# Kernel tuning notes

Measured on AMD Instinct MI355X. Metric: run time of the kernel, lower is better.

Reference implementation:

```python
import jax, jax.numpy as jnp
import numpy as np

B, S, D, H, HD = 2, 4096, 1024, 16, 64   # batch, seq, hidden, heads, head_dim
BLOCK, W = 64, 8                          # block size, local window in blocks (512 tokens)
ROPE_BASE = 10000.0


def _rope_tables(seq_len, dim, dtype):
    inv_freq = 1.0 / (ROPE_BASE ** (jnp.arange(0, dim, 2, dtype=jnp.float32) / dim))
    t = jnp.arange(seq_len, dtype=jnp.float32)
    freqs = jnp.einsum('i,j->ij', t, inv_freq)          # [S, dim/2]
    emb = jnp.concatenate([freqs, freqs], axis=-1)       # [S, dim]
    return jnp.cos(emb).astype(dtype), jnp.sin(emb).astype(dtype)


def _rotate_half(x):
    x1, x2 = x[..., : x.shape[-1] // 2], x[..., x.shape[-1] // 2:]
    return jnp.concatenate([-x2, x1], axis=-1)


def _apply_rope(q, k, position_ids):
    # q, k: [B, H, S, HD]; position_ids: [B, S]
    cos_t, sin_t = _rope_tables(S, HD, q.dtype)
    cos = cos_t[position_ids][:, None, :, :]             # [B, 1, S, HD]
    sin = sin_t[position_ids][:, None, :, :]
    q_emb = q * cos + _rotate_half(q) * sin
    k_emb = k * cos + _rotate_half(k) * sin
    return q_emb, k_emb


def _block_sparse_attention(q, k, v):
    # Causal block-sparse (sliding window of W blocks), DeepSpeed-style layout.
    # q, k, v: [B, H, S, HD]
    nb = S // BLOCK
    scale = 1.0 / jnp.sqrt(jnp.asarray(HD, q.dtype))
    qb = q.reshape(B, H, nb, BLOCK, HD)
    kb = k.reshape(B, H, nb, BLOCK, HD)
    vb = v.reshape(B, H, nb, BLOCK, HD)
    # block-column indices attended by each block-row: i-W+1 .. i
    idx = jnp.arange(nb)[:, None] - jnp.arange(W - 1, -1, -1)[None, :]   # [nb, W]
    valid = idx >= 0
    idxc = jnp.clip(idx, 0, nb - 1)
    kg = kb[:, :, idxc]                                   # [B, H, nb, W, BLOCK, HD]
    vg = vb[:, :, idxc]
    scores = jnp.einsum('bhnqd,bhnwkd->bhnqwk', qb, kg) * scale  # [B,H,nb,BLOCK,W,BLOCK]
    # absolute positions for causal mask within the window
    qpos = (jnp.arange(nb) * BLOCK)[:, None, None, None] + jnp.arange(BLOCK)[None, :, None, None]  # [nb,BLOCK,1,1]
    kpos = (idxc * BLOCK)[:, None, :, None] + jnp.arange(BLOCK)[None, None, None, :]               # [nb,1,W,BLOCK]
    mask = (kpos <= qpos) & valid[:, None, :, None]       # [nb, BLOCK, W, BLOCK]
    neg = jnp.asarray(-1e9, scores.dtype)
    scores = jnp.where(mask[None, None], scores, neg)
    scores = scores.reshape(B, H, nb, BLOCK, W * BLOCK)
    probs = jax.nn.softmax(scores, axis=-1)
    out = jnp.einsum('bhnqk,bhnkd->bhnqd', probs, vg.reshape(B, H, nb, W * BLOCK, HD))
    return out.reshape(B, H, S, HD)


def setup_inputs() -> dict:
    key = jax.random.key(0)
    ks = jax.random.split(key, 5)
    hidden_states = jax.random.normal(ks[0], (B, S, D), dtype=jnp.float32)
    position_ids = jnp.tile(jnp.arange(S, dtype=jnp.int32)[None, :], (B, 1))
    w_init = lambda k: (jax.random.normal(k, (D, D), dtype=jnp.float32) * 0.02)
    return {
        'hidden_states': hidden_states,
        'position_ids': position_ids,
        'wq': w_init(ks[1]),  # stored [in, out]
        'wk': w_init(ks[2]),
        'wv': w_init(ks[3]),
        'wo': w_init(ks[4]),
    }


def reference(hidden_states, position_ids, wq, wk, wv, wo):
    q = jnp.einsum('bsd,de->bse', hidden_states, wq).reshape(B, S, H, HD).transpose(0, 2, 1, 3)
    k = jnp.einsum('bsd,de->bse', hidden_states, wk).reshape(B, S, H, HD).transpose(0, 2, 1, 3)
    v = jnp.einsum('bsd,de->bse', hidden_states, wv).reshape(B, S, H, HD).transpose(0, 2, 1, 3)
    q, k = _apply_rope(q, k, position_ids)
    attn = _block_sparse_attention(q, k, v)               # [B, H, S, HD]
    attn = attn.transpose(0, 2, 1, 3).reshape(B, S, D)
    return jnp.einsum('bsd,de->bse', attn, wo)
```

## Files before the change

kernel.cpp:

```cpp
#include <hip/hip_runtime.h>
#include <cstdint>
#include <cstddef>

#define B_ 2
#define S_ 4096
#define D_ 1024
#define H_ 16
#define HD_ 64
#define NB_ 64
#define W_ 8
#define M_ (B_*S_)

#define QSCALE 0.18033688011112042f
#define LOG2_10000_OVER_32 0.41524101186092034f

typedef __bf16 bf16_t;
typedef __bf16 bf16x8 __attribute__((ext_vector_type(8)));
typedef float f32x4 __attribute__((ext_vector_type(4)));

#define GLOAD_LDS16(gp, lp) \
  __builtin_amdgcn_global_load_lds((__attribute__((address_space(1))) void*)(gp), \
                                   (__attribute__((address_space(3))) void*)(lp), 16, 0, 0)

__global__ void cast_bf16_kernel(const float* __restrict__ x, bf16_t* __restrict__ y, int n4) {
  int i = blockIdx.x * 256 + threadIdx.x;
  if (i >= n4) return;
  float4 v = ((const float4*)x)[i];
  union { bf16_t b[4]; uint2 u; } cv;
  cv.b[0] = (bf16_t)v.x; cv.b[1] = (bf16_t)v.y; cv.b[2] = (bf16_t)v.z; cv.b[3] = (bf16_t)v.w;
  ((uint2*)y)[i] = cv.u;
}

__global__ void transpose_cast_kernel(const float* __restrict__ w0, const float* __restrict__ w1,
                                      const float* __restrict__ w2, const float* __restrict__ w3,
                                      bf16_t* __restrict__ out) {
  const float* w = (blockIdx.z == 0) ? w0 : (blockIdx.z == 1) ? w1 : (blockIdx.z == 2) ? w2 : w3;
  bf16_t* wt = out + (size_t)blockIdx.z * D_ * D_;
  __shared__ float tile[32][33];
  int x = blockIdx.x * 32 + threadIdx.x;
  int y0 = blockIdx.y * 32;
  for (int i = threadIdx.y; i < 32; i += 8)
    tile[i][threadIdx.x] = w[(size_t)(y0 + i) * D_ + x];
  __syncthreads();
  int x2 = blockIdx.y * 32 + threadIdx.x;
  int y2 = blockIdx.x * 32;
  for (int i = threadIdx.y; i < 32; i += 8)
    wt[(size_t)(y2 + i) * D_ + x2] = (bf16_t)tile[threadIdx.x][i];
}

__global__ __launch_bounds__(512, 2) void gemm_qkv256(const bf16_t* __restrict__ A,
                                                      const bf16_t* __restrict__ Bt,
                                                      bf16_t* __restrict__ qkv,
                                                      bf16_t* __restrict__ vt_out,
                                                      const int* __restrict__ pos_ids) {
  const int bid = blockIdx.x;
  const int sid = (bid & 7) * 48 + (bid >> 3);
  const int mb = sid / 12, nb = sid % 12;
  const int mbase = mb * 256, nbase = nb * 256;
  const int tid = threadIdx.x;
  const int wid = tid >> 6, lane = tid & 63;
  const int quad = lane >> 4, l16 = lane & 15;
  const int wr = wid >> 2, wc = wid & 3;

  __shared__ bf16_t lds[4 * 16384];

  const int srow = wid * 16 + (lane >> 2);
  const int scol = (lane & 3) * 8;
  const bf16_t* gAb = A  + (size_t)(mbase + srow) * D_ + scol;
  const bf16_t* gBb = Bt + (size_t)(nbase + srow) * D_ + scol;

#define LDSA(b) (lds + (b) * 16384)
#define LDSB(b) (lds + (b) * 16384 + 8192)
#define STAGE_A(kt) do { bf16_t* p_ = LDSA((kt) & 3) + wid * 512; \
    GLOAD_LDS16(gAb + (kt) * 32, p_); \
    GLOAD_LDS16(gAb + (size_t)128 * D_ + (kt) * 32, p_ + 4096); } while (0)
#define STAGE_B(kt) do { bf16_t* p_ = LDSB((kt) & 3) + wid * 512; \
    GLOAD_LDS16(gBb + (kt) * 32, p_); \
    GLOAD_LDS16(gBb + (size_t)128 * D_ + (kt) * 32, p_ + 4096); } while (0)
#define WAITV(n) asm volatile("s_waitcnt vmcnt(" #n ")" ::: "memory")
#define BAR() do { __builtin_amdgcn_s_barrier(); asm volatile("" ::: "memory"); } while (0)

  f32x4 acc[8][4];
#pragma unroll
  for (int m = 0; m < 8; ++m)
#pragma unroll
    for (int n = 0; n < 4; ++n) acc[m][n] = (f32x4){0.f, 0.f, 0.f, 0.f};

#define PHASE(kt, mh, STG, WT) do { \
    const bf16_t* Ab_ = LDSA((kt) & 3); \
    const bf16_t* Bb_ = LDSB((kt) & 3); \
    bf16x8 af_[4], bf_[4]; \
    _Pragma("unroll") \
    for (int m = 0; m < 4; ++m) \
      af_[m] = *(const bf16x8*)&Ab_[(wr * 128 + (mh) * 64 + m * 16 + l16) * 32 + quad * 8]; \
    _Pragma("unroll") \
    for (int n = 0; n < 4; ++n) \
      bf_[n] = *(const bf16x8*)&Bb_[(wc * 64 + n * 16 + l16) * 32 + quad * 8]; \
    STG; WT; \
    BAR(); \
    __builtin_amdgcn_s_setprio(1); \
    _Pragma("unroll") \
    for (int m = 0; m < 4; ++m) \
      _Pragma("unroll") \
      for (int n = 0; n < 4; ++n) \
        acc[(mh) * 4 + m][n] = \
            __builtin_amdgcn_mfma_f32_16x16x32_bf16(af_[m], bf_[n], acc[(mh) * 4 + m][n], 0, 0, 0); \
    __builtin_amdgcn_s_setprio(0); \
    BAR(); \
  } while (0)

  STAGE_A(0); STAGE_B(0); STAGE_A(1); STAGE_B(1); STAGE_A(2); STAGE_B(2);
  WAITV(8);
  BAR();

  for (int kt = 0; kt < 29; ++kt) {
    PHASE(kt, 0, STAGE_A(kt + 3), (void)0);
    PHASE(kt, 1, STAGE_B(kt + 3), WAITV(8));
  }
  PHASE(29, 0, (void)0, (void)0);
  PHASE(29, 1, (void)0, WAITV(4));
  PHASE(30, 0, (void)0, (void)0);
  PHASE(30, 1, (void)0, WAITV(0));
  PHASE(31, 0, (void)0, (void)0);
  PHASE(31, 1, (void)0, (void)0);

  const int zsl = nb >> 2;
  if (zsl < 2) {
    bf16_t* Cp = qkv + (size_t)zsl * M_ * D_;
    const float qsc = (zsl == 0) ? QSCALE : 1.0f;
    float invf[2];
#pragma unroll
    for (int ni = 0; ni < 2; ++ni)
      invf[ni] = __builtin_exp2f(-(float)(ni * 16 + l16) * LOG2_10000_OVER_32);
    const int colb = (nb & 3) * 256 + wc * 64;
#pragma unroll
    for (int m = 0; m < 8; ++m) {
#pragma unroll
      for (int r = 0; r < 4; ++r) {
        int row = mbase + wr * 128 + m * 16 + quad * 4 + r;
        float fpos = (float)pos_ids[row];
#pragma unroll
        for (int ni = 0; ni < 2; ++ni) {
          float sn, cs;
          __sincosf(fpos * invf[ni], &sn, &cs);
          float x1 = acc[m][ni][r], x2 = acc[m][ni + 2][r];
          int col = colb + ni * 16 + l16;
          Cp[(size_t)row * D_ + col]      = (bf16_t)((x1 * cs - x2 * sn) * qsc);
          Cp[(size_t)row * D_ + col + 32] = (bf16_t)((x2 * cs + x1 * sn) * qsc);
        }
      }
    }
  } else {
    const int h = (nb & 3) * 4 + wc;
#pragma unroll
    for (int mh = 0; mh < 2; ++mh) {
      int rowblk = mb * 4 + wr * 2 + mh;
      int bb = rowblk >> 6, sblk = rowblk & 63;
      size_t vbase = (size_t)(bb * H_ + h) * HD_ * S_;
#pragma unroll
      for (int n = 0; n < 4; ++n) {
        int d = n * 16 + l16;
        union { bf16_t bv[16]; uint4 u[2]; } pk;
#pragma unroll
        for (int r = 0; r < 4; ++r)
#pragma unroll
          for (int mi = 0; mi < 4; ++mi)
            pk.bv[r * 4 + mi] = (bf16_t)acc[mh * 4 + mi][n][r];
        size_t addr = vbase + (size_t)d * S_ + (size_t)sblk * 64 + quad * 16;
        *(uint4*)&vt_out[addr]     = pk.u[0];
        *(uint4*)&vt_out[addr + 8] = pk.u[1];
      }
    }
  }
#undef PHASE
#undef STAGE_A
#undef STAGE_B
#undef LDSA
#undef LDSB
#undef WAITV
#undef BAR
}

template<bool OBF>
__global__ __launch_bounds__(256) void gemm128(const bf16_t* __restrict__ A,
                                               const bf16_t* __restrict__ BtBase,
                                               void* __restrict__ Cbase,
                                               bf16_t* __restrict__ vt_out,
                                               const int* __restrict__ pos_ids) {
  const bf16_t* Bt = BtBase + (size_t)blockIdx.z * D_ * D_;
  const int mb = blockIdx.y * 128, nb = blockIdx.x * 128;
  const int tid = threadIdx.x;
  const int wid = tid >> 6, lane = tid & 63;
  const int quad = lane >> 4, l16 = lane & 15;
  const int wr = wid >> 1, wc = wid & 1;

  __shared__ bf16_t As[128 * 32];
  __shared__ bf16_t Bs[128 * 32];

  f32x4 acc[4][4];
#pragma unroll
  for (int mi = 0; mi < 4; ++mi)
#pragma unroll
    for (int ni = 0; ni < 4; ++ni)
      acc[mi][ni] = (f32x4){0.f, 0.f, 0.f, 0.f};

  const int acol = (lane & 3) * 8;
  const int arow0 = wid * 32 + (lane >> 2);
  const bf16_t* gA = A + (size_t)(mb + arow0) * D_ + acol;
  const bf16_t* gB = Bt + (size_t)(nb + arow0) * D_ + acol;

  for (int kt = 0; kt < 32; ++kt) {
    const int k0 = kt * 32;
    __syncthreads();
#pragma unroll
    for (int c = 0; c < 2; ++c) {
      GLOAD_LDS16(gA + (size_t)c * 16 * D_ + k0, As + (wid * 2 + c) * 512);
      GLOAD_LDS16(gB + (size_t)c * 16 * D_ + k0, Bs + (wid * 2 + c) * 512);
    }
    __syncthreads();
    bf16x8 af[4], bfr[4];
#pragma unroll
    for (int mi = 0; mi < 4; ++mi)
      af[mi] = *(const bf16x8*)&As[(wr * 64 + mi * 16 + l16) * 32 + quad * 8];
#pragma unroll
    for (int ni = 0; ni < 4; ++ni)
      bfr[ni] = *(const bf16x8*)&Bs[(wc * 64 + ni * 16 + l16) * 32 + quad * 8];
#pragma unroll
    for (int mi = 0; mi < 4; ++mi)
#pragma unroll
      for (int ni = 0; ni < 4; ++ni)
        acc[mi][ni] = __builtin_amdgcn_mfma_f32_16x16x32_bf16(af[mi], bfr[ni], acc[mi][ni], 0, 0, 0);
  }

  if constexpr (OBF) {
  } else {
    float* Cp = (float*)Cbase;
#pragma unroll
    for (int mi = 0; mi < 4; ++mi)
#pragma unroll
      for (int ni = 0; ni < 4; ++ni)
#pragma unroll
        for (int r = 0; r < 4; ++r) {
          int row = mb + wr * 64 + mi * 16 + quad * 4 + r;
          int col = nb + wc * 64 + ni * 16 + l16;
          Cp[(size_t)row * D_ + col] = acc[mi][ni][r];
        }
  }
}

__global__ __launch_bounds__(256) void attn_kernel(const bf16_t* __restrict__ q,
                                                   const bf16_t* __restrict__ k,
                                                   const bf16_t* __restrict__ vt,
                                                   bf16_t* __restrict__ o) {
  const int m = blockIdx.x, h = blockIdx.y, b = blockIdx.z;
  const int n0 = m * 2, n1 = n0 + 1;
  const int tid = threadIdx.x;
  const int wid = tid >> 6, lane = tid & 63;
  const int quad = lane >> 4, l16 = lane & 15;

  __shared__ bf16_t Ks[64 * 72];
  __shared__ bf16_t Vs[64 * 72];
  __shared__ bf16_t Ps[4][16 * 72];

  const size_t hoff = (size_t)h * HD_;
  const size_t vtbase = (size_t)(b * H_ + h) * HD_ * S_;
  const size_t rowb[2] = {(size_t)(b * S_ + n0 * 64), (size_t)(b * S_ + n1 * 64)};

  bf16x8 aq[2][2];
#pragma unroll
  for (int x = 0; x < 2; ++x) {
    const bf16_t* qr = q + (rowb[x] + wid * 16 + l16) * D_ + hoff;
    aq[x][0] = *(const bf16x8*)(qr + quad * 8);
    aq[x][1] = *(const bf16x8*)(qr + 32 + quad * 8);
  }

  f32x4 o_acc[2][4];
  float lsum[2][4];
#pragma unroll
  for (int x = 0; x < 2; ++x)
#pragma unroll
    for (int t = 0; t < 4; ++t) {
      o_acc[x][t] = (f32x4){0.f, 0.f, 0.f, 0.f};
      lsum[x][t] = 0.f;
    }

  const int srow = tid >> 3;
  const int scol = (tid & 7) * 8;

  const int kb0 = (n0 >= W_ - 1) ? n0 - (W_ - 1) : 0;
  for (int kb = kb0; kb <= n1; ++kb) {
    __syncthreads();
    const size_t krow = (size_t)(b * S_ + kb * 64);
#pragma unroll
    for (int it = 0; it < 2; ++it) {
      int r = it * 32 + srow;
      *(uint4*)&Ks[r * 72 + scol] = *(const uint4*)&k[(krow + r) * D_ + hoff + scol];
      *(uint4*)&Vs[r * 72 + scol] = *(const uint4*)&vt[vtbase + (size_t)r * S_ + kb * 64 + scol];
    }
    __syncthreads();

#pragma unroll
    for (int x = 0; x < 2; ++x) {
      const int nx = n0 + x;
      if (x == 0 ? (kb > n0) : (kb < n1 - (W_ - 1))) continue;

      f32x4 sacc[4];
#pragma unroll
      for (int t = 0; t < 4; ++t) sacc[t] = (f32x4){0.f, 0.f, 0.f, 0.f};
#pragma unroll
      for (int t = 0; t < 4; ++t) {
        bf16x8 bk0 = *(const bf16x8*)&Ks[(t * 16 + l16) * 72 + quad * 8];
        bf16x8 bk1 = *(const bf16x8*)&Ks[(t * 16 + l16) * 72 + 32 + quad * 8];
        sacc[t] = __builtin_amdgcn_mfma_f32_16x16x32_bf16(aq[x][0], bk0, sacc[t], 0, 0, 0);
        sacc[t] = __builtin_amdgcn_mfma_f32_16x16x32_bf16(aq[x][1], bk1, sacc[t], 0, 0, 0);
      }

      const bool diag = (kb == nx);
#pragma unroll
      for (int r = 0; r < 4; ++r) {
        int qpos = wid * 16 + quad * 4 + r;
        union { bf16_t bv[4]; uint2 u; } pk;
        float rs = 0.f;
#pragma unroll
        for (int t = 0; t < 4; ++t) {
          float p = __builtin_exp2f(sacc[t][r]);
          if (diag && (t * 16 + l16 > qpos)) p = 0.f;
          rs += p;
          pk.bv[t] = (bf16_t)p;
        }
        lsum[x][r] += rs;
        *(uint2*)&Ps[wid][(quad * 4 + r) * 72 + l16 * 4] = pk.u;
      }

      bf16x8 pa0 = *(const bf16x8*)&Ps[wid][l16 * 72 + quad * 8];
      bf16x8 pa1 = *(const bf16x8*)&Ps[wid][l16 * 72 + 32 + quad * 8];
#pragma unroll
      for (int t = 0; t < 4; ++t) {
        bf16x8 vb0 = *(const bf16x8*)&Vs[(t * 16 + l16) * 72 + quad * 8];
        bf16x8 vb1 = *(const bf16x8*)&Vs[(t * 16 + l16) * 72 + 32 + quad * 8];
        o_acc[x][t] = __builtin_amdgcn_mfma_f32_16x16x32_bf16(pa0, vb0, o_acc[x][t], 0, 0, 0);
        o_acc[x][t] = __builtin_amdgcn_mfma_f32_16x16x32_bf16(pa1, vb1, o_acc[x][t], 0, 0, 0);
      }
    }
  }

#pragma unroll
  for (int x = 0; x < 2; ++x) {
    float inv[4];
#pragma unroll
    for (int r = 0; r < 4; ++r) {
      float s = lsum[x][r];
#pragma unroll
      for (int off = 1; off < 16; off <<= 1) s += __shfl_xor(s, off);
      inv[r] = 1.f / s;
    }
#pragma unroll
    for (int t = 0; t < 4; ++t)
#pragma unroll
      for (int r = 0; r < 4; ++r) {
        int row = wid * 16 + quad * 4 + r;
        int col = t * 16 + l16;
        o[(rowb[x] + row) * D_ + hoff + col] = (bf16_t)(o_acc[x][t][r] * inv[r]);
      }
  }
}

extern "C" void kernel_launch(void* const* d_in, const int* in_sizes, int n_in,
                              void* d_out, int out_size, void* d_ws, size_t ws_size,
                              hipStream_t stream) {
  const float* hs = (const float*)d_in[0];
  const int* pos  = (const int*)d_in[1];
  const float* wq = (const float*)d_in[2];
  const float* wk = (const float*)d_in[3];
  const float* wv = (const float*)d_in[4];
  const float* wo = (const float*)d_in[5];

  bf16_t* ws   = (bf16_t*)d_ws;
  bf16_t* hsb  = ws;
  bf16_t* wT   = hsb + (size_t)M_ * D_;
  bf16_t* qkv  = wT + (size_t)4 * D_ * D_;
  bf16_t* attn = qkv + (size_t)3 * M_ * D_;
  bf16_t* qw  = qkv;
  bf16_t* kw  = qkv + (size_t)M_ * D_;
  bf16_t* vtg = qkv + (size_t)2 * M_ * D_;

  cast_bf16_kernel<<<(M_ * D_ / 4 + 255) / 256, 256, 0, stream>>>(hs, hsb, M_ * D_ / 4);
  transpose_cast_kernel<<<dim3(D_ / 32, D_ / 32, 4), dim3(32, 8), 0, stream>>>(wq, wk, wv, wo, wT);
  gemm_qkv256<<<dim3(384), dim3(512), 0, stream>>>(hsb, wT, qkv, vtg, pos);
  attn_kernel<<<dim3(NB_ / 2, H_, B_), 256, 0, stream>>>(qw, kw, vtg, attn);
  gemm128<false><<<dim3(D_ / 128, M_ / 128, 1), 256, 0, stream>>>(attn, wT + (size_t)3 * D_ * D_, d_out, nullptr, pos);
}
```

Measured before the change: 253.2 us.

## XOR-swizzle GEMM LDS layout and merge half-phases into one barrier per k-tile

Both GEMM kernels now permute the 16-byte k-chunk each lane writes through global_load_lds by XOR with row bits, and read fragments with the matching swizzled index. The goal is to cut LDS bank conflicts on the 64-byte-stride row reads. The QKV GEMM also fuses its two half-M phases into one phase per k-tile, loading all 8 A fragments and issuing 32 MFMAs between barriers. This halves the number of barriers, at the cost of more live fragment registers, which could affect occupancy under launch_bounds(512,2).

```diff
diff --git a/kernel.cpp b/kernel.cpp
--- a/kernel.cpp
+++ b/kernel.cpp
@@ -65,9 +65,10 @@
   __shared__ bf16_t lds[4 * 16384];
 
   const int srow = wid * 16 + (lane >> 2);
-  const int scol = (lane & 3) * 8;
-  const bf16_t* gAb = A  + (size_t)(mbase + srow) * D_ + scol;
-  const bf16_t* gBb = Bt + (size_t)(nbase + srow) * D_ + scol;
+  const int schunk = (lane & 3) ^ ((lane >> 3) & 3);
+  const bf16_t* gAb = A  + (size_t)(mbase + srow) * D_ + schunk * 8;
+  const bf16_t* gBb = Bt + (size_t)(nbase + srow) * D_ + schunk * 8;
+  const int quadx = (quad ^ ((l16 >> 1) & 3)) * 8;
 
 #define LDSA(b) (lds + (b) * 16384)
 #define LDSB(b) (lds + (b) * 16384 + 8192)
@@ -86,26 +87,25 @@
 #pragma unroll
     for (int n = 0; n < 4; ++n) acc[m][n] = (f32x4){0.f, 0.f, 0.f, 0.f};
 
-#define PHASE(kt, mh, STG, WT) do { \
+#define PHASE(kt, STG, WT) do { \
     const bf16_t* Ab_ = LDSA((kt) & 3); \
     const bf16_t* Bb_ = LDSB((kt) & 3); \
-    bf16x8 af_[4], bf_[4]; \
+    bf16x8 af_[8], bf_[4]; \
     _Pragma("unroll") \
-    for (int m = 0; m < 4; ++m) \
-      af_[m] = *(const bf16x8*)&Ab_[(wr * 128 + (mh) * 64 + m * 16 + l16) * 32 + quad * 8]; \
+    for (int m = 0; m < 8; ++m) \
+      af_[m] = *(const bf16x8*)&Ab_[(wr * 128 + m * 16 + l16) * 32 + quadx]; \
     _Pragma("unroll") \
     for (int n = 0; n < 4; ++n) \
-      bf_[n] = *(const bf16x8*)&Bb_[(wc * 64 + n * 16 + l16) * 32 + quad * 8]; \
-    STG; WT; \
-    BAR(); \
+      bf_[n] = *(const bf16x8*)&Bb_[(wc * 64 + n * 16 + l16) * 32 + quadx]; \
+    STG; \
     __builtin_amdgcn_s_setprio(1); \
     _Pragma("unroll") \
-    for (int m = 0; m < 4; ++m) \
+    for (int m = 0; m < 8; ++m) \
       _Pragma("unroll") \
       for (int n = 0; n < 4; ++n) \
-        acc[(mh) * 4 + m][n] = \
-            __builtin_amdgcn_mfma_f32_16x16x32_bf16(af_[m], bf_[n], acc[(mh) * 4 + m][n], 0, 0, 0); \
+        acc[m][n] = __builtin_amdgcn_mfma_f32_16x16x32_bf16(af_[m], bf_[n], acc[m][n], 0, 0, 0); \
     __builtin_amdgcn_s_setprio(0); \
+    WT; \
     BAR(); \
   } while (0)
 
@@ -113,16 +113,11 @@
   WAITV(8);
   BAR();
 
-  for (int kt = 0; kt < 29; ++kt) {
-    PHASE(kt, 0, STAGE_A(kt + 3), (void)0);
-    PHASE(kt, 1, STAGE_B(kt + 3), WAITV(8));
-  }
-  PHASE(29, 0, (void)0, (void)0);
-  PHASE(29, 1, (void)0, WAITV(4));
-  PHASE(30, 0, (void)0, (void)0);
-  PHASE(30, 1, (void)0, WAITV(0));
-  PHASE(31, 0, (void)0, (void)0);
-  PHASE(31, 1, (void)0, (void)0);
+  for (int kt = 0; kt < 29; ++kt)
+    PHASE(kt, ({ STAGE_A(kt + 3); STAGE_B(kt + 3); }), WAITV(8));
+  PHASE(29, (void)0, WAITV(4));
+  PHASE(30, (void)0, WAITV(0));
+  PHASE(31, (void)0, (void)0);
 
   const int zsl = nb >> 2;
   if (zsl < 2) {
@@ -204,8 +199,9 @@
     for (int ni = 0; ni < 4; ++ni)
       acc[mi][ni] = (f32x4){0.f, 0.f, 0.f, 0.f};
 
-  const int acol = (lane & 3) * 8;
+  const int acol = ((lane & 3) ^ ((lane >> 3) & 3)) * 8;
   const int arow0 = wid * 32 + (lane >> 2);
+  const int quadx = (quad ^ ((l16 >> 1) & 3)) * 8;
   const bf16_t* gA = A + (size_t)(mb + arow0) * D_ + acol;
   const bf16_t* gB = Bt + (size_t)(nb + arow0) * D_ + acol;
 
@@ -221,10 +217,10 @@
     bf16x8 af[4], bfr[4];
 #pragma unroll
     for (int mi = 0; mi < 4; ++mi)
-      af[mi] = *(const bf16x8*)&As[(wr * 64 + mi * 16 + l16) * 32 + quad * 8];
+      af[mi] = *(const bf16x8*)&As[(wr * 64 + mi * 16 + l16) * 32 + quadx];
 #pragma unroll
     for (int ni = 0; ni < 4; ++ni)
-      bfr[ni] = *(const bf16x8*)&Bs[(wc * 64 + ni * 16 + l16) * 32 + quad * 8];
+      bfr[ni] = *(const bf16x8*)&Bs[(wc * 64 + ni * 16 + l16) * 32 + quadx];
 #pragma unroll
     for (int mi = 0; mi < 4; ++mi)
 #pragma unroll
```

Measured after the change: 243.0 us. -4.0%, faster.
